# Kernel tuning notes

Hardware: AMD Instinct MI355X
Metric: run time of the kernel (lower is better)

## Reference

```python
import jax, jax.numpy as jnp
import numpy as np

K_ORDER = 4
BETA = 0.5
NUM_HEADS = 1
IN_CHANNELS = 128


def _gcn_conv(x, row, col, values, N):
    # x: [N, H, D]; symmetric-normalized scatter-add message passing
    deg = jax.ops.segment_sum(values, row, num_segments=N)            # [N]
    dinv = jnp.where(deg > 0, deg ** -0.5, jnp.zeros_like(deg))
    coef = dinv[row] * dinv[col] * values                             # [E]
    return jax.ops.segment_sum(x[col] * coef[:, None, None], row, num_segments=N)


def _fast_attn_conv(qs, ks, vs, batch, pos, n_nodes_f, B, max_node):
    # qs/ks/vs: [N, H, D]; ragged graphs padded to [B, max_node, H, D]
    N, H, D = vs.shape
    q_pad = jnp.zeros((B, max_node, H, D), qs.dtype).at[batch, pos].set(qs)
    k_pad = jnp.zeros((B, max_node, H, D), ks.dtype).at[batch, pos].set(ks)
    v_pad = jnp.zeros((B, max_node, H, D), vs.dtype).at[batch, pos].set(vs)
    qk = jnp.einsum('bmhd,bnhd->bmhn', q_pad, k_pad)                  # [B, M, H, M]
    v_sum = jax.ops.segment_sum(vs, batch, num_segments=B)            # [B, H, D]
    numer_pad = jnp.einsum('bmhn,bnhd->bmhd', qk, v_pad)              # [B, M, H, D]
    numer = numer_pad[batch, pos] + v_sum[batch]                      # [N, H, D]
    denom = qk[batch, pos].sum(-1) + n_nodes_f[batch][:, None]        # [N, H]
    return numer / denom[..., None]


def _forward(x, edge_weight, Wq_w, Wq_b, Wk_w, Wk_b, Wo_w, Wo_b,
             row, col, batch, pos, n_nodes_f, B, max_node):
    N, C = x.shape
    H = NUM_HEADS
    query = (x @ Wq_w.T + Wq_b).reshape(N, H, C)
    key = (x @ Wk_w.T + Wk_b).reshape(N, H, C)
    qs = query / jnp.linalg.norm(query, axis=2, keepdims=True)
    ks = key / jnp.linalg.norm(key, axis=2, keepdims=True)
    cur = jnp.broadcast_to(x[:, None, :], (N, H, C))                  # x_0
    acc = cur
    for _ in range(K_ORDER):
        gcn_i = _gcn_conv(cur, row, col, edge_weight, N)
        attn_i = _fast_attn_conv(qs, ks, cur, batch, pos, n_nodes_f, B, max_node)
        cur = BETA * gcn_i + (1.0 - BETA) * attn_i
        acc = acc + cur
    out = acc.reshape(N, H * C) @ Wo_w.T + Wo_b
    return out / H


def setup_inputs():
    key = jax.random.key(0)
    k = jax.random.split(key, 10)
    B, per_graph = 64, 512
    N = B * per_graph
    C, H, OUT = IN_CHANNELS, NUM_HEADS, 128
    E = N * 16
    s = 1.0 / np.sqrt(C)
    return {
        'x': jax.random.normal(k[0], (N, C), jnp.float32),
        'edge_index': jax.random.randint(k[1], (2, E), 0, N, jnp.int32),
        'edge_weight': jax.random.uniform(k[2], (E,), jnp.float32),
        'n_nodes': jnp.full((B,), per_graph, jnp.int32),
        'Wq_w': jax.random.uniform(k[3], (H * C, C), jnp.float32, -s, s),
        'Wq_b': jax.random.uniform(k[4], (H * C,), jnp.float32, -s, s),
        'Wk_w': jax.random.uniform(k[5], (H * C, C), jnp.float32, -s, s),
        'Wk_b': jax.random.uniform(k[6], (H * C,), jnp.float32, -s, s),
        'Wo_w': jax.random.uniform(k[7], (OUT, H * C), jnp.float32, -s, s),
        'Wo_b': jax.random.uniform(k[8], (OUT,), jnp.float32, -s, s),
    }


def reference(x, edge_index, edge_weight, n_nodes, Wq_w, Wq_b, Wk_w, Wk_b, Wo_w, Wo_b):
    n_np = np.asarray(n_nodes)
    B, max_node = n_np.shape[0], int(n_np.max())
    N = x.shape[0]
    batch = jnp.asarray(np.repeat(np.arange(B), n_np))                # [N] graph id per node
    offsets = jnp.asarray(np.concatenate([[0], np.cumsum(n_np)[:-1]]))
    pos = jnp.arange(N) - offsets[batch]                              # within-graph index
    n_nodes_f = jnp.asarray(n_np, jnp.float32)
    row, col = edge_index[0], edge_index[1]
    return _forward(x, edge_weight, Wq_w, Wq_b, Wk_w, Wk_b, Wo_w, Wo_b,
                    row, col, batch, pos, n_nodes_f, B, max_node)
```

## Files before the change

### kernel.cpp

```cpp
#include <hip/hip_runtime.h>
#include <stdint.h>

#define C 128

typedef __attribute__((ext_vector_type(8))) short bfrag;
typedef __attribute__((ext_vector_type(4))) float ffrag;

__device__ __forceinline__ unsigned short f2bf(float f){
  union { float f; unsigned int i; } v; v.f = f;
  unsigned int x = v.i;
  unsigned int r = x + 0x7fffu + ((x >> 16) & 1u);
  return (unsigned short)(r >> 16);
}
__device__ __forceinline__ float bf2f(unsigned short u){
  union { unsigned int i; float f; } v; v.i = ((unsigned int)u) << 16; return v.f;
}

__global__ void k_zero_region(unsigned int* base, int nwords){
  int i = blockIdx.x * 256 + threadIdx.x;
  if (i < nwords) base[i] = 0u;
}

__global__ void k_degcast(const int* __restrict__ row, const float* __restrict__ w,
                          unsigned long long* deg64, int* __restrict__ rank, int E,
                          const float* __restrict__ Wq, const float* __restrict__ Wk,
                          const float* __restrict__ Wo, unsigned short* __restrict__ W16,
                          int WW, int degB){
  int bx = blockIdx.x;
  if (bx < degB){
    int e = bx * 256 + threadIdx.x;
    if (e < E){
      int r = row[e];
      unsigned int wf = (unsigned int)(w[e] * 16777216.0f + 0.5f);
      unsigned long long old =
          atomicAdd(&deg64[r], 0x100000000ULL | (unsigned long long)wf);
      rank[e] = (int)(old >> 32);
    }
  } else {
    int i = (bx - degB) * 256 + threadIdx.x;
    if (i < 3 * WW){
      const float* src = (i < WW) ? Wq : ((i < 2 * WW) ? Wk : Wo);
      int off = (i < WW) ? 0 : ((i < 2 * WW) ? WW : 2 * WW);
      W16[i] = f2bf(src[i - off]);
    }
  }
}

__global__ void k_scan1(const unsigned long long* __restrict__ deg64,
                        float* __restrict__ dinv, int* bsum, int N){
  __shared__ int s[256];
  int b = blockIdx.x, t = threadIdx.x;
  int i = b * 256 + t;
  int cnt = 0;
  if (i < N){
    unsigned long long v = deg64[i];
    cnt = (int)(v >> 32);
    unsigned int lo = (unsigned int)v;
    float d = (float)lo * (1.0f / 16777216.0f);
    dinv[i] = lo > 0u ? 1.0f / sqrtf(d) : 0.f;
  }
  s[t] = cnt;
  __syncthreads();
  for (int o = 128; o; o >>= 1){ if (t < o) s[t] += s[t + o]; __syncthreads(); }
  if (t == 0) bsum[b] = s[0];
}

__global__ void k_scan3(const unsigned long long* __restrict__ deg64,
                        const int* __restrict__ bsum, int* row_ptr, int N){
  __shared__ int s[256];
  int b = blockIdx.x, t = threadIdx.x;
  int i = b * 256 + t;
  int v = (i < N) ? (int)(deg64[i] >> 32) : 0;
  s[t] = v;
  __syncthreads();
  for (int o = 1; o < 256; o <<= 1){
    int u = (t >= o) ? s[t - o] : 0;
    __syncthreads(); s[t] += u; __syncthreads();
  }
  int base = 0;
  for (int j = 0; j < b; j++) base += bsum[j];
  int excl = base + s[t] - v;
  if (i < N) row_ptr[i] = excl;
  if (i == N - 1) row_ptr[N] = excl + v;
}

__global__ __launch_bounds__(256) void k_fillprep(
    const int* __restrict__ row, const int* __restrict__ col,
    const float* __restrict__ w, const int* __restrict__ rank,
    const int* __restrict__ row_ptr, const float* __restrict__ dinv,
    int2* __restrict__ edge_s, int E, int fillB,
    const float* __restrict__ x, unsigned short* __restrict__ cur0,
    unsigned short* __restrict__ curT, int N){
  __shared__ unsigned short tile[64][66];
  int bx = blockIdx.x;
  if (bx < fillB){
    int e = bx * 256 + threadIdx.x;
    if (e < E){
      int r = row[e], c = col[e];
      int p = row_ptr[r] + rank[e];
      float cf = dinv[r] * dinv[c] * w[e];
      int2 ed; ed.x = c; ed.y = __float_as_int(cf);
      edge_s[p] = ed;
    }
    return;
  }
  int pb = bx - fillB;
  int ntiles = N >> 6;
  int n0 = (pb % ntiles) * 64;
  int c0 = (pb / ntiles) * 64;
  int tx = threadIdx.x & 63, ty = threadIdx.x >> 6;
  for (int r = ty; r < 64; r += 4){
    float v = x[(size_t)(n0 + r) * C + c0 + tx];
    unsigned short u = f2bf(v);
    cur0[(size_t)(n0 + r) * C + c0 + tx] = u;
    tile[r][tx] = u;
  }
  __syncthreads();
  for (int r = ty; r < 64; r += 4)
    curT[(size_t)(c0 + r) * N + n0 + tx] = tile[tx][r];
}

__global__ __launch_bounds__(256) void k_proj2(const unsigned short* __restrict__ x,
      const unsigned short* __restrict__ W16,
      const float* __restrict__ Wq_b, const float* __restrict__ Wk_b,
      unsigned short* __restrict__ qs, unsigned short* __restrict__ ksT,
      int N, int wblocks){
  int bx = blockIdx.x;
  int transposed = bx >= wblocks;
  int lb = transposed ? bx - wblocks : bx;
  const unsigned short* W = transposed ? (W16 + C * C) : W16;
  const float* Wb = transposed ? Wk_b : Wq_b;
  unsigned short* out = transposed ? ksT : qs;

  int wv = threadIdx.x >> 6, l = threadIdx.x & 63;
  int m0 = (lb * 4 + wv) * 16;
  if (m0 >= N) return;
  int quad = l >> 4, lcol = l & 15;
  ffrag acc[8] = {};
  const unsigned short* Abase = x + (size_t)(m0 + lcol) * C + quad * 8;
#pragma unroll
  for (int s = 0; s < 4; s++){
    bfrag a = *(const bfrag*)(Abase + s * 32);
#pragma unroll
    for (int nt = 0; nt < 8; nt++){
      bfrag bb = *(const bfrag*)(W + (size_t)(nt * 16 + lcol) * C + s * 32 + quad * 8);
      acc[nt] = __builtin_amdgcn_mfma_f32_16x16x32_bf16(a, bb, acc[nt], 0, 0, 0);
    }
  }
  float q[8][4];
  float ss[4] = {0.f, 0.f, 0.f, 0.f};
#pragma unroll
  for (int nt = 0; nt < 8; nt++){
    float bias = Wb[nt * 16 + lcol];
#pragma unroll
    for (int r = 0; r < 4; r++){ float v = acc[nt][r] + bias; q[nt][r] = v; ss[r] += v * v; }
  }
#pragma unroll
  for (int off = 1; off < 16; off <<= 1){
#pragma unroll
    for (int r = 0; r < 4; r++) ss[r] += __shfl_xor(ss[r], off, 64);
  }
  float inv[4];
#pragma unroll
  for (int r = 0; r < 4; r++) inv[r] = 1.0f / sqrtf(fmaxf(ss[r], 1e-30f));
  if (!transposed){
#pragma unroll
    for (int nt = 0; nt < 8; nt++)
#pragma unroll
      for (int r = 0; r < 4; r++)
        out[(size_t)(m0 + quad * 4 + r) * C + nt * 16 + lcol] = f2bf(q[nt][r] * inv[r]);
  } else {
#pragma unroll
    for (int nt = 0; nt < 8; nt++){
      ushort4 pk;
      pk.x = f2bf(q[nt][0] * inv[0]); pk.y = f2bf(q[nt][1] * inv[1]);
      pk.z = f2bf(q[nt][2] * inv[2]); pk.w = f2bf(q[nt][3] * inv[3]);
      *(ushort4*)(out + (size_t)(nt * 16 + lcol) * N + m0 + quad * 4) = pk;
    }
  }
}

__global__ void k_denom(const unsigned short* __restrict__ qs, const float* __restrict__ ksum,
                        const int* __restrict__ n_nodes, float* denom, int N, int PG){
  int wv = threadIdx.x >> 6, l = threadIdx.x & 63;
  int m = blockIdx.x * 4 + wv;
  if (m >= N) return;
  int b = m / PG;
  float s = bf2f(qs[(size_t)m * C + l]) * ksum[b * C + l]
          + bf2f(qs[(size_t)m * C + 64 + l]) * ksum[b * C + 64 + l];
#pragma unroll
  for (int off = 32; off; off >>= 1) s += __shfl_xor(s, off, 64);
  if (l == 0) denom[m] = s + (float)n_nodes[b];
}

__global__ __launch_bounds__(256) void k_mid(const unsigned short* __restrict__ ksT,
      const unsigned short* __restrict__ curT, unsigned short* __restrict__ MT,
      const int* __restrict__ row_ptr, const int2* __restrict__ edge_s,
      const unsigned int* __restrict__ cur32, unsigned int* __restrict__ gcn32,
      float* __restrict__ vsum, float* __restrict__ ksum,
      int N, int PG, int mB, int vsB, int ksB, int gcnB){
  int bx = blockIdx.x;
  if (bx < mB){
    int wv = threadIdx.x >> 6, l = threadIdx.x & 63;
    int b = bx >> 2;
    int gw = (bx & 3) * 4 + wv;
    int itile = gw & 7, jh = gw >> 3;
    int quad = l >> 4, lcol = l & 15;
    ffrag acc[4] = {};
    const unsigned short* Arow = ksT + (size_t)(itile * 16 + lcol) * N + (size_t)b * PG + quad * 8;
    const unsigned short* B0 = curT + (size_t)b * PG + quad * 8;
    int steps = PG / 32;
    for (int s = 0; s < steps; s++){
      bfrag a = *(const bfrag*)(Arow + s * 32);
#pragma unroll
      for (int jt = 0; jt < 4; jt++){
        bfrag bb = *(const bfrag*)(B0 + (size_t)((jh * 4 + jt) * 16 + lcol) * N + s * 32);
        acc[jt] = __builtin_amdgcn_mfma_f32_16x16x32_bf16(a, bb, acc[jt], 0, 0, 0);
      }
    }
    unsigned short* MTb = MT + (size_t)b * C * C;
    int i0 = itile * 16 + quad * 4;
#pragma unroll
    for (int jt = 0; jt < 4; jt++){
      int j = (jh * 4 + jt) * 16 + lcol;
      ushort4 pk;
      pk.x = f2bf(acc[jt][0]); pk.y = f2bf(acc[jt][1]);
      pk.z = f2bf(acc[jt][2]); pk.w = f2bf(acc[jt][3]);
      *(ushort4*)(MTb + (size_t)j * C + i0) = pk;
    }
    return;
  }
  bx -= mB;
  if (bx < vsB + ksB){
    const unsigned short* src = (bx < vsB) ? curT : ksT;
    float* dst = (bx < vsB) ? vsum : ksum;
    int b = (bx < vsB) ? bx : (bx - vsB);
    int wv = threadIdx.x >> 6, l = threadIdx.x & 63;
    for (int d = wv * 32; d < wv * 32 + 32; d++){
      float s = 0.f;
      for (int n0 = l * 8; n0 < PG; n0 += 512){
        bfrag v = *(const bfrag*)(src + (size_t)d * N + (size_t)b * PG + n0);
#pragma unroll
        for (int j = 0; j < 8; j++) s += bf2f((unsigned short)v[j]);
      }
#pragma unroll
      for (int off = 32; off; off >>= 1) s += __shfl_xor(s, off, 64);
      if (l == 0) dst[b * C + d] = s;
    }
    return;
  }
  bx -= vsB + ksB;
  if (bx < gcnB){
    int nid = bx * 4 + (threadIdx.x >> 6);
    int c = threadIdx.x & 63;
    if (nid >= N) return;
    int s = row_ptr[nid], e = row_ptr[nid + 1];
    float a0 = 0.f, a1 = 0.f;
    int p = s;
    for (; p + 4 <= e; p += 4){
      int2 e0 = edge_s[p],     e1 = edge_s[p + 1];
      int2 e2 = edge_s[p + 2], e3 = edge_s[p + 3];
      float f0 = __int_as_float(e0.y), f1 = __int_as_float(e1.y);
      float f2 = __int_as_float(e2.y), f3 = __int_as_float(e3.y);
      unsigned int u0 = cur32[(size_t)e0.x * 64 + c];
      unsigned int u1 = cur32[(size_t)e1.x * 64 + c];
      unsigned int u2 = cur32[(size_t)e2.x * 64 + c];
      unsigned int u3 = cur32[(size_t)e3.x * 64 + c];
      a0 += f0 * bf2f((unsigned short)(u0 & 0xffffu));
      a1 += f0 * bf2f((unsigned short)(u0 >> 16));
      a0 += f1 * bf2f((unsigned short)(u1 & 0xffffu));
      a1 += f1 * bf2f((unsigned short)(u1 >> 16));
      a0 += f2 * bf2f((unsigned short)(u2 & 0xffffu));
      a1 += f2 * bf2f((unsigned short)(u2 >> 16));
      a0 += f3 * bf2f((unsigned short)(u3 & 0xffffu));
      a1 += f3 * bf2f((unsigned short)(u3 >> 16));
    }
    for (; p < e; p++){
      int2 ed = edge_s[p];
      float cf = __int_as_float(ed.y);
      unsigned int u = cur32[(size_t)ed.x * 64 + c];
      a0 += cf * bf2f((unsigned short)(u & 0xffffu));
      a1 += cf * bf2f((unsigned short)(u >> 16));
    }
    gcn32[(size_t)nid * 64 + c] = ((unsigned int)f2bf(a1) << 16) | (unsigned int)f2bf(a0);
  }
}

__global__ __launch_bounds__(256) void k_phase2(const unsigned short* __restrict__ qs,
      const unsigned short* __restrict__ MT, const float* __restrict__ vsum,
      const float* __restrict__ denom, const unsigned short* __restrict__ gcn16,
      unsigned short* __restrict__ curO, unsigned short* __restrict__ curT,
      int N, int PG){
  int wv = threadIdx.x >> 6, l = threadIdx.x & 63;
  int m0 = (blockIdx.x * 4 + wv) * 16;
  if (m0 >= N) return;
  int b = m0 / PG;
  int quad = l >> 4, lcol = l & 15;
  ffrag acc[8] = {};
  const unsigned short* Abase = qs + (size_t)(m0 + lcol) * C + quad * 8;
  const unsigned short* MTb = MT + (size_t)b * C * C;
#pragma unroll
  for (int s = 0; s < 4; s++){
    bfrag a = *(const bfrag*)(Abase + s * 32);
#pragma unroll
    for (int dt = 0; dt < 8; dt++){
      bfrag bb = *(const bfrag*)(MTb + (size_t)(dt * 16 + lcol) * C + s * 32 + quad * 8);
      acc[dt] = __builtin_amdgcn_mfma_f32_16x16x32_bf16(a, bb, acc[dt], 0, 0, 0);
    }
  }
  float dn[4];
#pragma unroll
  for (int r = 0; r < 4; r++) dn[r] = denom[m0 + quad * 4 + r];
#pragma unroll
  for (int dt = 0; dt < 8; dt++){
    int d = dt * 16 + lcol;
    float vs = vsum[b * C + d];
    ushort4 pk;
#pragma unroll
    for (int r = 0; r < 4; r++){
      int m = m0 + quad * 4 + r;
      float attn = (acc[dt][r] + vs) / dn[r];
      float g = bf2f(gcn16[(size_t)m * C + d]);
      unsigned short nb = f2bf(0.5f * (g + attn));
      curO[(size_t)m * C + d] = nb;
      ((unsigned short*)&pk)[r] = nb;
    }
    *(ushort4*)(curT + (size_t)d * N + m0 + quad * 4) = pk;
  }
}

__global__ __launch_bounds__(256) void k_final(const float* __restrict__ x,
      const unsigned short* __restrict__ c1, const unsigned short* __restrict__ c2,
      const unsigned short* __restrict__ c3, const unsigned short* __restrict__ c4,
      const unsigned short* __restrict__ Wo, const float* __restrict__ Wob,
      float* __restrict__ out, int N){
  int wv = threadIdx.x >> 6, l = threadIdx.x & 63;
  int m0 = (blockIdx.x * 4 + wv) * 16;
  if (m0 >= N) return;
  int quad = l >> 4, lcol = l & 15;
  ffrag acc[8] = {};
  size_t rowoff = (size_t)(m0 + lcol) * C + quad * 8;
#pragma unroll
  for (int s = 0; s < 4; s++){
    size_t base = rowoff + s * 32;
    float4 xa0 = *(const float4*)(x + base);
    float4 xa1 = *(const float4*)(x + base + 4);
    bfrag b1 = *(const bfrag*)(c1 + base);
    bfrag b2 = *(const bfrag*)(c2 + base);
    bfrag b3 = *(const bfrag*)(c3 + base);
    bfrag b4 = *(const bfrag*)(c4 + base);
    float xs[8] = {xa0.x, xa0.y, xa0.z, xa0.w, xa1.x, xa1.y, xa1.z, xa1.w};
    bfrag a;
#pragma unroll
    for (int j = 0; j < 8; j++){
      float v = (((xs[j] + bf2f((unsigned short)b1[j])) + bf2f((unsigned short)b2[j]))
                 + bf2f((unsigned short)b3[j])) + bf2f((unsigned short)b4[j]);
      a[j] = (short)f2bf(v);
    }
#pragma unroll
    for (int ot = 0; ot < 8; ot++){
      bfrag bb = *(const bfrag*)(Wo + (size_t)(ot * 16 + lcol) * C + s * 32 + quad * 8);
      acc[ot] = __builtin_amdgcn_mfma_f32_16x16x32_bf16(a, bb, acc[ot], 0, 0, 0);
    }
  }
#pragma unroll
  for (int ot = 0; ot < 8; ot++){
    float bias = Wob[ot * 16 + lcol];
#pragma unroll
    for (int r = 0; r < 4; r++){
      out[(size_t)(m0 + quad * 4 + r) * C + ot * 16 + lcol] = acc[ot][r] + bias;
    }
  }
}


extern "C" void kernel_launch(void* const* d_in, const int* in_sizes, int n_in,
                              void* d_out, int out_size, void* d_ws, size_t ws_size,
                              hipStream_t stream){
  const float* x    = (const float*)d_in[0];
  const int*   eidx = (const int*)d_in[1];
  const float* ew   = (const float*)d_in[2];
  const int*   n_nodes = (const int*)d_in[3];
  const float* Wq_w = (const float*)d_in[4];
  const float* Wq_b = (const float*)d_in[5];
  const float* Wk_w = (const float*)d_in[6];
  const float* Wk_b = (const float*)d_in[7];
  const float* Wo_w = (const float*)d_in[8];
  const float* Wo_b = (const float*)d_in[9];
  float* out = (float*)d_out;

  int N = in_sizes[0] / C;
  int E = in_sizes[2];
  int B = in_sizes[3];
  int PG = N / B;
  int BC = B * C;
  const int* row = eidx;
  const int* col = eidx + E;

  char* p = (char*)d_ws;
  auto alloc = [&](size_t bytes) -> void* {
    void* r = (void*)p; p += (bytes + 255) & ~(size_t)255; return r;
  };
  unsigned short* cur[5];
  for (int i = 0; i < 5; i++) cur[i] = (unsigned short*)alloc((size_t)N * C * 2);
  unsigned short* curT  = (unsigned short*)alloc((size_t)N * C * 2);
  unsigned short* qs16  = (unsigned short*)alloc((size_t)N * C * 2);
  unsigned short* ksT   = (unsigned short*)alloc((size_t)N * C * 2);
  unsigned short* gcn16 = (unsigned short*)alloc((size_t)N * C * 2);
  unsigned short* MT    = (unsigned short*)alloc((size_t)B * C * C * 2);
  unsigned short* W16   = (unsigned short*)alloc((size_t)3 * C * C * 2);
  unsigned long long* deg64 = (unsigned long long*)alloc((size_t)N * 8);
  float*          dinv  = (float*)alloc((size_t)N * 4);
  int*            row_ptr = (int*)alloc((size_t)(N + 1) * 4);
  int*            rank  = (int*)alloc((size_t)E * 4);
  int*            bsum  = (int*)alloc(1024);
  int2*           edge_s = (int2*)alloc((size_t)E * 8);
  float*          ksum  = (float*)alloc((size_t)BC * 4);
  float*          vsum  = (float*)alloc((size_t)BC * 4);
  float*          denom = (float*)alloc((size_t)N * 4);

  dim3 b256(256);
  int wblocks = (N / 16 + 3) / 4;
  int WW = C * C;
  int nscan = (N + 255) / 256;
  int degB = (E + 255) / 256;
  int castB = (3 * WW + 255) / 256;
  int fillB = (E + 255) / 256;
  int prepB = (N / 64) * (C / 64);
  int mB = 4 * B;
  int gcnB = (N + 3) / 4;
  int vsB = B;

  k_zero_region<<<dim3((2 * N + 255) / 256), b256, 0, stream>>>((unsigned int*)deg64, 2 * N);
  k_degcast<<<dim3(degB + castB), b256, 0, stream>>>(row, ew, deg64, rank, E,
                                                     Wq_w, Wk_w, Wo_w, W16, WW, degB);
  k_scan1<<<dim3(nscan), b256, 0, stream>>>(deg64, dinv, bsum, N);
  k_scan3<<<dim3(nscan), b256, 0, stream>>>(deg64, bsum, row_ptr, N);
  k_fillprep<<<dim3(fillB + prepB), b256, 0, stream>>>(row, col, ew, rank, row_ptr, dinv,
                                                       edge_s, E, fillB,
                                                       x, cur[0], curT, N);
  k_proj2<<<dim3(2 * wblocks), b256, 0, stream>>>(cur[0], W16, Wq_b, Wk_b,
                                                  qs16, ksT, N, wblocks);

  for (int it = 0; it < 4; it++){
    int ksB = (it == 0) ? B : 0;
    k_mid<<<dim3(mB + vsB + ksB + gcnB), b256, 0, stream>>>(ksT, curT, MT, row_ptr, edge_s,
                                                      (const unsigned int*)cur[it],
                                                      (unsigned int*)gcn16,
                                                      vsum, ksum,
                                                      N, PG, mB, vsB, ksB, gcnB);
    if (it == 0)
      k_denom<<<dim3((N + 3) / 4), b256, 0, stream>>>(qs16, ksum, n_nodes, denom, N, PG);
    k_phase2<<<dim3(wblocks), b256, 0, stream>>>(qs16, MT, vsum, denom, gcn16,
                                                 cur[it + 1], curT, N, PG);
  }

  k_final<<<dim3(wblocks), b256, 0, stream>>>(x, cur[1], cur[2], cur[3], cur[4],
                                              W16 + 2 * WW, Wo_b, out, N);
}
```

Before: 386.0 us.

## Merge prep kernels and fold denominator computation into first phase2 pass

Moves the x-to-bf16 cast and transpose into the degree/weight-cast kernel, and merges the q/k projection into the edge-fill kernel, so independent work shares launches. The separate denominator kernel is removed. The first phase2 iteration now computes q·ksum from its already-loaded A fragments, reduces it with shuffles and stores it for later iterations. This cuts two kernel launches and a re-read of qs, at the cost of extra work and branching inside phase2 on the first iteration.

```diff
diff --git a/kernel.cpp b/kernel.cpp
--- a/kernel.cpp
+++ b/kernel.cpp
@@ -21,11 +21,14 @@
   if (i < nwords) base[i] = 0u;
 }
 
-__global__ void k_degcast(const int* __restrict__ row, const float* __restrict__ w,
-                          unsigned long long* deg64, int* __restrict__ rank, int E,
-                          const float* __restrict__ Wq, const float* __restrict__ Wk,
-                          const float* __restrict__ Wo, unsigned short* __restrict__ W16,
-                          int WW, int degB){
+__global__ __launch_bounds__(256) void k_prep1(
+    const int* __restrict__ row, const float* __restrict__ w,
+    unsigned long long* deg64, int* __restrict__ rank, int E, int degB,
+    const float* __restrict__ x, unsigned short* __restrict__ cur0,
+    unsigned short* __restrict__ curT, int N, int prepB,
+    const float* __restrict__ Wq, const float* __restrict__ Wk,
+    const float* __restrict__ Wo, unsigned short* __restrict__ W16, int WW){
+  __shared__ unsigned short tile[64][66];
   int bx = blockIdx.x;
   if (bx < degB){
     int e = bx * 256 + threadIdx.x;
@@ -36,13 +39,31 @@
           atomicAdd(&deg64[r], 0x100000000ULL | (unsigned long long)wf);
       rank[e] = (int)(old >> 32);
     }
-  } else {
-    int i = (bx - degB) * 256 + threadIdx.x;
-    if (i < 3 * WW){
-      const float* src = (i < WW) ? Wq : ((i < 2 * WW) ? Wk : Wo);
-      int off = (i < WW) ? 0 : ((i < 2 * WW) ? WW : 2 * WW);
-      W16[i] = f2bf(src[i - off]);
-    }
+    return;
+  }
+  bx -= degB;
+  if (bx < prepB){
+    int ntiles = N >> 6;
+    int n0 = (bx % ntiles) * 64;
+    int c0 = (bx / ntiles) * 64;
+    int tx = threadIdx.x & 63, ty = threadIdx.x >> 6;
+    for (int r = ty; r < 64; r += 4){
+      float v = x[(size_t)(n0 + r) * C + c0 + tx];
+      unsigned short u = f2bf(v);
+      cur0[(size_t)(n0 + r) * C + c0 + tx] = u;
+      tile[r][tx] = u;
+    }
+    __syncthreads();
+    for (int r = ty; r < 64; r += 4)
+      curT[(size_t)(c0 + r) * N + n0 + tx] = tile[tx][r];
+    return;
+  }
+  bx -= prepB;
+  int i = bx * 256 + threadIdx.x;
+  if (i < 3 * WW){
+    const float* src = (i < WW) ? Wq : ((i < 2 * WW) ? Wk : Wo);
+    int off = (i < WW) ? 0 : ((i < 2 * WW) ? WW : 2 * WW);
+    W16[i] = f2bf(src[i - off]);
   }
 }
 
@@ -84,14 +105,15 @@
   if (i == N - 1) row_ptr[N] = excl + v;
 }
 
-__global__ __launch_bounds__(256) void k_fillprep(
+__global__ __launch_bounds__(256) void k_prep2(
     const int* __restrict__ row, const int* __restrict__ col,
     const float* __restrict__ w, const int* __restrict__ rank,
     const int* __restrict__ row_ptr, const float* __restrict__ dinv,
     int2* __restrict__ edge_s, int E, int fillB,
-    const float* __restrict__ x, unsigned short* __restrict__ cur0,
-    unsigned short* __restrict__ curT, int N){
-  __shared__ unsigned short tile[64][66];
+    const unsigned short* __restrict__ x, const unsigned short* __restrict__ W16,
+    const float* __restrict__ Wq_b, const float* __restrict__ Wk_b,
+    unsigned short* __restrict__ qs, unsigned short* __restrict__ ksT,
+    int N, int wblocks){
   int bx = blockIdx.x;
   if (bx < fillB){
     int e = bx * 256 + threadIdx.x;
@@ -104,28 +126,7 @@
     }
     return;
   }
-  int pb = bx - fillB;
-  int ntiles = N >> 6;
-  int n0 = (pb % ntiles) * 64;
-  int c0 = (pb / ntiles) * 64;
-  int tx = threadIdx.x & 63, ty = threadIdx.x >> 6;
-  for (int r = ty; r < 64; r += 4){
-    float v = x[(size_t)(n0 + r) * C + c0 + tx];
-    unsigned short u = f2bf(v);
-    cur0[(size_t)(n0 + r) * C + c0 + tx] = u;
-    tile[r][tx] = u;
-  }
-  __syncthreads();
-  for (int r = ty; r < 64; r += 4)
-    curT[(size_t)(c0 + r) * N + n0 + tx] = tile[tx][r];
-}
-
-__global__ __launch_bounds__(256) void k_proj2(const unsigned short* __restrict__ x,
-      const unsigned short* __restrict__ W16,
-      const float* __restrict__ Wq_b, const float* __restrict__ Wk_b,
-      unsigned short* __restrict__ qs, unsigned short* __restrict__ ksT,
-      int N, int wblocks){
-  int bx = blockIdx.x;
+  bx -= fillB;
   int transposed = bx >= wblocks;
   int lb = transposed ? bx - wblocks : bx;
   const unsigned short* W = transposed ? (W16 + C * C) : W16;
@@ -178,19 +179,6 @@
       *(ushort4*)(out + (size_t)(nt * 16 + lcol) * N + m0 + quad * 4) = pk;
     }
   }
-}
-
-__global__ void k_denom(const unsigned short* __restrict__ qs, const float* __restrict__ ksum,
-                        const int* __restrict__ n_nodes, float* denom, int N, int PG){
-  int wv = threadIdx.x >> 6, l = threadIdx.x & 63;
-  int m = blockIdx.x * 4 + wv;
-  if (m >= N) return;
-  int b = m / PG;
-  float s = bf2f(qs[(size_t)m * C + l]) * ksum[b * C + l]
-          + bf2f(qs[(size_t)m * C + 64 + l]) * ksum[b * C + 64 + l];
-#pragma unroll
-  for (int off = 32; off; off >>= 1) s += __shfl_xor(s, off, 64);
-  if (l == 0) denom[m] = s + (float)n_nodes[b];
 }
 
 __global__ __launch_bounds__(256) void k_mid(const unsigned short* __restrict__ ksT,
@@ -288,9 +276,10 @@
 
 __global__ __launch_bounds__(256) void k_phase2(const unsigned short* __restrict__ qs,
       const unsigned short* __restrict__ MT, const float* __restrict__ vsum,
-      const float* __restrict__ denom, const unsigned short* __restrict__ gcn16,
+      const float* __restrict__ ksum, const int* __restrict__ n_nodes,
+      float* __restrict__ denom, const unsigned short* __restrict__ gcn16,
       unsigned short* __restrict__ curO, unsigned short* __restrict__ curT,
-      int N, int PG){
+      int N, int PG, int it0){
   int wv = threadIdx.x >> 6, l = threadIdx.x & 63;
   int m0 = (blockIdx.x * 4 + wv) * 16;
   if (m0 >= N) return;
@@ -299,9 +288,16 @@
   ffrag acc[8] = {};
   const unsigned short* Abase = qs + (size_t)(m0 + lcol) * C + quad * 8;
   const unsigned short* MTb = MT + (size_t)b * C * C;
+  const float* ksb = ksum + b * C;
+  float dsum = 0.f;
 #pragma unroll
   for (int s = 0; s < 4; s++){
     bfrag a = *(const bfrag*)(Abase + s * 32);
+    if (it0){
+#pragma unroll
+      for (int j = 0; j < 8; j++)
+        dsum += bf2f((unsigned short)a[j]) * ksb[quad * 8 + s * 32 + j];
+    }
 #pragma unroll
     for (int dt = 0; dt < 8; dt++){
       bfrag bb = *(const bfrag*)(MTb + (size_t)(dt * 16 + lcol) * C + s * 32 + quad * 8);
@@ -309,8 +305,17 @@
     }
   }
   float dn[4];
-#pragma unroll
-  for (int r = 0; r < 4; r++) dn[r] = denom[m0 + quad * 4 + r];
+  if (it0){
+    dsum += __shfl_xor(dsum, 16, 64);
+    dsum += __shfl_xor(dsum, 32, 64);
+    float dfull = dsum + (float)n_nodes[b];
+    if (quad == 0) denom[m0 + lcol] = dfull;
+#pragma unroll
+    for (int r = 0; r < 4; r++) dn[r] = __shfl(dfull, quad * 4 + r, 64);
+  } else {
+#pragma unroll
+    for (int r = 0; r < 4; r++) dn[r] = denom[m0 + quad * 4 + r];
+  }
 #pragma unroll
   for (int dt = 0; dt < 8; dt++){
     int d = dt * 16 + lcol;
@@ -432,15 +437,15 @@
   int vsB = B;
 
   k_zero_region<<<dim3((2 * N + 255) / 256), b256, 0, stream>>>((unsigned int*)deg64, 2 * N);
-  k_degcast<<<dim3(degB + castB), b256, 0, stream>>>(row, ew, deg64, rank, E,
-                                                     Wq_w, Wk_w, Wo_w, W16, WW, degB);
+  k_prep1<<<dim3(degB + prepB + castB), b256, 0, stream>>>(row, ew, deg64, rank, E, degB,
+                                                           x, cur[0], curT, N, prepB,
+                                                           Wq_w, Wk_w, Wo_w, W16, WW);
   k_scan1<<<dim3(nscan), b256, 0, stream>>>(deg64, dinv, bsum, N);
   k_scan3<<<dim3(nscan), b256, 0, stream>>>(deg64, bsum, row_ptr, N);
-  k_fillprep<<<dim3(fillB + prepB), b256, 0, stream>>>(row, col, ew, rank, row_ptr, dinv,
-                                                       edge_s, E, fillB,
-                                                       x, cur[0], curT, N);
-  k_proj2<<<dim3(2 * wblocks), b256, 0, stream>>>(cur[0], W16, Wq_b, Wk_b,
-                                                  qs16, ksT, N, wblocks);
+  k_prep2<<<dim3(fillB + 2 * wblocks), b256, 0, stream>>>(row, col, ew, rank, row_ptr, dinv,
+                                                          edge_s, E, fillB,
+                                                          cur[0], W16, Wq_b, Wk_b,
+                                                          qs16, ksT, N, wblocks);
 
   for (int it = 0; it < 4; it++){
     int ksB = (it == 0) ? B : 0;
@@ -449,10 +454,9 @@
                                                       (unsigned int*)gcn16,
                                                       vsum, ksum,
                                                       N, PG, mB, vsB, ksB, gcnB);
-    if (it == 0)
-      k_denom<<<dim3((N + 3) / 4), b256, 0, stream>>>(qs16, ksum, n_nodes, denom, N, PG);
-    k_phase2<<<dim3(wblocks), b256, 0, stream>>>(qs16, MT, vsum, denom, gcn16,
-                                                 cur[it + 1], curT, N, PG);
+    k_phase2<<<dim3(wblocks), b256, 0, stream>>>(qs16, MT, vsum, ksum, n_nodes, denom,
+                                                 gcn16, cur[it + 1], curT,
+                                                 N, PG, (it == 0) ? 1 : 0);
   }
 
   k_final<<<dim3(wblocks), b256, 0, stream>>>(x, cur[1], cur[2], cur[3], cur[4],
```

New measurement: 381.8 us. About the same (-1.1%).
